# Kernel tuning notes

Hardware: AMD Instinct MI355X
Metric: run time of the kernel (lower is better)

The kernel has to match this reference:

```python
import jax, jax.numpy as jnp
import numpy as np
import math

NUM_HEADS = 16


def setup_inputs() -> dict:
    key = jax.random.key(0)
    ks = jax.random.split(key, 5)
    B, C, H = 2, 2048, 1024
    return {
        "x": jax.random.normal(ks[0], (B, C, H), dtype=jnp.float32),
        "Wqkv_w": jax.random.normal(ks[1], (3 * H, H), dtype=jnp.float32) * (1.0 / math.sqrt(H)),
        "Wqkv_b": jax.random.normal(ks[2], (3 * H,), dtype=jnp.float32) * 0.02,
        "Wo_w": jax.random.normal(ks[3], (H, H), dtype=jnp.float32) * (1.0 / math.sqrt(H)),
        "Wo_b": jax.random.normal(ks[4], (H,), dtype=jnp.float32) * 0.02,
    }


def reference(x, Wqkv_w, Wqkv_b, Wo_w, Wo_b):
    B, C, H = x.shape
    nh = NUM_HEADS
    hd = H // nh
    # QKV projection (torch Linear: x @ W.T + b)
    qkv = x @ Wqkv_w.T + Wqkv_b                      # [B, C, 3H]
    qkv = qkv.reshape(B, C, 3, nh, hd)
    qkv = jnp.transpose(qkv, (2, 0, 3, 1, 4))        # [3, B, nh, C, hd]
    q, k, v = qkv[0], qkv[1], qkv[2]
    scale = 1.0 / math.sqrt(hd)
    att = jnp.einsum('bhqd,bhkd->bhqk', q, k) * scale  # [B, nh, C, C]
    causal = jnp.triu(jnp.ones((C, C), dtype=bool), k=1)  # True above diagonal
    att = jnp.where(causal[None, None], jnp.float32(-jnp.inf), att)
    att = jax.nn.softmax(att, axis=-1)
    # dropout p set to 0 (eval-mode math)
    out = jnp.einsum('bhqk,bhkd->bhqd', att, v)       # [B, nh, C, hd]
    out = jnp.transpose(out, (0, 2, 1, 3)).reshape(B, C, H)
    return out @ Wo_w.T + Wo_b
```

## Files before the change

### kernel.cpp

```cpp
#include <hip/hip_runtime.h>
#include <hip/hip_bf16.h>
#include <math.h>

typedef unsigned short u16;
typedef __attribute__((ext_vector_type(8))) __bf16 bf16x8;
typedef __attribute__((ext_vector_type(4))) float f32x4;
typedef __attribute__((ext_vector_type(8))) unsigned short u16x8;
typedef __attribute__((ext_vector_type(4))) unsigned int u32x4;

__device__ __forceinline__ u16 f2bf(float f) {
  union { float f; unsigned u; } x; x.f = f;
  unsigned r = x.u + 0x7fffu + ((x.u >> 16) & 1u);
  return (u16)(r >> 16);
}

__device__ __forceinline__ void gload16(const u16* g, u16* l) {
  __builtin_amdgcn_global_load_lds(
      (const __attribute__((address_space(1))) void*)g,
      (__attribute__((address_space(3))) void*)l, 16, 0, 0);
}

#define MFMA16(a, b, c) __builtin_amdgcn_mfma_f32_16x16x32_bf16((a), (b), (c), 0, 0, 0)

#define QSCALE 0.18033688011112043f

__global__ __launch_bounds__(256) void cast_all_kernel(
    const float* __restrict__ x, const float* __restrict__ wqkv,
    const float* __restrict__ wo, u16* __restrict__ xb,
    u16* __restrict__ wqb, u16* __restrict__ wob) {
  int i = blockIdx.x * 256 + threadIdx.x;
  const float* src; u16* dst;
  if (i < 1048576)      { src = x;    dst = xb;  }
  else if (i < 1835008) { src = wqkv; dst = wqb; i -= 1048576; }
  else                  { src = wo;   dst = wob; i -= 1835008; }
  f32x4 v = *(const f32x4*)(src + (size_t)i * 4);
  u16 o0 = f2bf(v[0]), o1 = f2bf(v[1]), o2 = f2bf(v[2]), o3 = f2bf(v[3]);
  unsigned lo = (unsigned)o0 | ((unsigned)o1 << 16);
  unsigned hi = (unsigned)o2 | ((unsigned)o3 << 16);
  ((unsigned*)dst)[(size_t)i * 2] = lo;
  ((unsigned*)dst)[(size_t)i * 2 + 1] = hi;
}

__global__ __launch_bounds__(512, 2) void gemm_qkv_kernel(
    const u16* __restrict__ X, const u16* __restrict__ W, const float* __restrict__ bias,
    u16* __restrict__ Qb, u16* __restrict__ Kb, u16* __restrict__ Vb) {
  __shared__ __align__(16) u16 As[2][2][128 * 64];
  __shared__ __align__(16) u16 Bs[2][2][128 * 64];
  const int tid = threadIdx.x;
  const int lane = tid & 63;
  const int wid = tid >> 6;
  const int wm = wid >> 2, wn = wid & 3;
  const int g = lane >> 4, q15 = lane & 15;
  const int m0b = blockIdx.y * 256;
  const int n0b = blockIdx.x * 256;
  const int sA = 2 * ((q15 >> 2) & 1);

  auto stageA = [&](int kt, int h) {
    #pragma unroll
    for (int it = 0; it < 2; ++it) {
      int c = it * 512 + tid;
      int row = c >> 3, kg = c & 7;
      int kgs = kg ^ (2 * ((row >> 2) & 1));
      gload16(X + (size_t)(m0b + h * 128 + row) * 1024 + kt * 64 + kgs * 8,
              &As[kt & 1][h][c * 8]);
    }
  };
  auto stageB = [&](int kt, int h) {
    #pragma unroll
    for (int it = 0; it < 2; ++it) {
      int c = it * 512 + tid;
      int row = c >> 3, kg = c & 7;
      int kgs = kg ^ (2 * ((row >> 2) & 1));
      gload16(W + (size_t)(n0b + h * 128 + row) * 1024 + kt * 64 + kgs * 8,
              &Bs[kt & 1][h][c * 8]);
    }
  };

  f32x4 acc[8][4] = {};

  stageA(0, 0); stageA(0, 1);
  stageB(0, 0); stageB(0, 1);
  stageB(1, 0); stageB(1, 1);
  asm volatile("s_waitcnt vmcnt(4)" ::: "memory");
  __builtin_amdgcn_s_barrier();

  for (int kt = 0; kt < 16; ++kt) {
    const int d = kt & 1;
    const u16* Ah = As[d][wm];
    const u16* Bh = Bs[d][wn >> 1];
    const int rB0 = (wn & 1) * 64;
    bf16x8 bfr[4][2];
    #pragma unroll
    for (int q = 0; q < 4; ++q) {
      bf16x8 afr[2][2];
      if (q == 0) {
        #pragma unroll
        for (int n = 0; n < 4; ++n)
          #pragma unroll
          for (int kk = 0; kk < 2; ++kk) {
            int row = rB0 + n * 16 + q15;
            int kg = (kk * 4 + g) ^ sA;
            bfr[n][kk] = *(const bf16x8*)(Bh + row * 64 + kg * 8);
          }
      }
      #pragma unroll
      for (int p = 0; p < 2; ++p)
        #pragma unroll
        for (int kk = 0; kk < 2; ++kk) {
          int row = (2 * q + p) * 16 + q15;
          int kg = (kk * 4 + g) ^ sA;
          afr[p][kk] = *(const bf16x8*)(Ah + row * 64 + kg * 8);
        }
      if (q == 0)      { if (kt + 1 < 16) stageA(kt + 1, 0); }
      else if (q == 1) { if (kt + 1 < 16) stageA(kt + 1, 1); }
      else if (q == 2) { if (kt + 2 < 16) stageB(kt + 2, 0); }
      else             { if (kt + 2 < 16) stageB(kt + 2, 1); }
      __builtin_amdgcn_s_barrier();
      asm volatile("s_waitcnt lgkmcnt(0)" ::: "memory");
      __builtin_amdgcn_sched_barrier(0);
      __builtin_amdgcn_s_setprio(1);
      #pragma unroll
      for (int kk = 0; kk < 2; ++kk)
        #pragma unroll
        for (int p = 0; p < 2; ++p)
          #pragma unroll
          for (int n = 0; n < 4; ++n)
            acc[2 * q + p][n] = MFMA16(afr[p][kk], bfr[n][kk], acc[2 * q + p][n]);
      __builtin_amdgcn_s_setprio(0);
      if (q == 3) {
        if (kt < 14)       asm volatile("s_waitcnt vmcnt(4)" ::: "memory");
        else if (kt == 14) asm volatile("s_waitcnt vmcnt(0)" ::: "memory");
      }
      __builtin_amdgcn_s_barrier();
    }
  }

  const int which = n0b >> 10;
  const float qs = (which == 0) ? QSCALE : 1.0f;
  u16* __restrict__ dst = (which == 0) ? Qb : (which == 1 ? Kb : Vb);
  #pragma unroll
  for (int n = 0; n < 4; ++n) {
    int gcol = n0b + wn * 64 + n * 16 + q15;
    float bz = bias[gcol];
    int h = (gcol >> 6) & 15, d0 = gcol & 63;
    #pragma unroll
    for (int m = 0; m < 8; ++m)
      #pragma unroll
      for (int j = 0; j < 4; ++j) {
        int grow = m0b + wm * 128 + m * 16 + g * 4 + j;
        int bb = grow >> 11, qq = grow & 2047;
        dst[((size_t)((bb * 16 + h) * 2048 + qq)) * 64 + d0] =
            f2bf((acc[m][n][j] + bz) * qs);
      }
  }
}

__global__ __launch_bounds__(256) void gemm_out_kernel(
    const u16* __restrict__ Ain, const u16* __restrict__ W, const float* __restrict__ bias,
    float* __restrict__ out) {
  __shared__ __align__(16) u16 As[64 * 64];
  __shared__ __align__(16) u16 Bs[128 * 64];
  const int tid = threadIdx.x;
  const int lane = tid & 63;
  const int wc = tid >> 6;
  const int m0 = blockIdx.y * 64;
  const int n0 = blockIdx.x * 128;
  f32x4 acc[4][2] = {};
  for (int k0 = 0; k0 < 1024; k0 += 64) {
    #pragma unroll
    for (int it = 0; it < 2; ++it) {
      int c = it * 256 + tid;
      gload16(Ain + (size_t)(m0 + (c >> 3)) * 1024 + k0 + ((c & 7) << 3), As + c * 8);
    }
    #pragma unroll
    for (int it = 0; it < 4; ++it) {
      int c = it * 256 + tid;
      gload16(W + (size_t)(n0 + (c >> 3)) * 1024 + k0 + ((c & 7) << 3), Bs + c * 8);
    }
    __syncthreads();
    #pragma unroll
    for (int kk = 0; kk < 2; ++kk) {
      bf16x8 a[4], b[2];
      #pragma unroll
      for (int m = 0; m < 4; ++m)
        a[m] = *(const bf16x8*)(As + ((m * 16 + (lane & 15)) * 64 +
                                      kk * 32 + ((lane >> 4) << 3)));
      #pragma unroll
      for (int n = 0; n < 2; ++n)
        b[n] = *(const bf16x8*)(Bs + ((wc * 32 + n * 16 + (lane & 15)) * 64 +
                                      kk * 32 + ((lane >> 4) << 3)));
      #pragma unroll
      for (int m = 0; m < 4; ++m)
        #pragma unroll
        for (int n = 0; n < 2; ++n)
          acc[m][n] = MFMA16(a[m], b[n], acc[m][n]);
    }
    __syncthreads();
  }
  #pragma unroll
  for (int m = 0; m < 4; ++m)
    #pragma unroll
    for (int n = 0; n < 2; ++n)
      #pragma unroll
      for (int j = 0; j < 4; ++j) {
        int row = m0 + m * 16 + ((lane >> 4) << 2) + j;
        int col = n0 + wc * 32 + n * 16 + (lane & 15);
        out[(size_t)row * 1024 + col] = acc[m][n][j] + bias[col];
      }
}

__device__ __forceinline__ void attn_one(
    const u16* __restrict__ Qh, const u16* __restrict__ Kh, const u16* __restrict__ Vh,
    u16* __restrict__ Ob, int bb, int h, int qt,
    u16 (*Ks)[64 * 64], u16 (*Vt)[64 * 64]) {
  const int tid = threadIdx.x, lane = tid & 63, w = tid >> 6;
  const int g = lane >> 4, q15 = lane & 15;

  bf16x8 qf[2];
  const int qrow = qt * 64 + w * 16 + q15;
  #pragma unroll
  for (int kk = 0; kk < 2; ++kk)
    qf[kk] = *(const bf16x8*)(Qh + (size_t)qrow * 64 + kk * 32 + g * 8);

  f32x4 acc_o[4];
  #pragma unroll
  for (int n = 0; n < 4; ++n) acc_o[n] = (f32x4){0.f, 0.f, 0.f, 0.f};
  float m_run = -INFINITY, l_run = 0.f;

  const int nt = qt + 1;

  auto stageK = [&](int t, int buf) {
    #pragma unroll
    for (int it = 0; it < 2; ++it) {
      int c = it * 256 + tid;
      int row = c >> 3, b8 = c & 7;
      gload16(Kh + (size_t)(t * 64 + row) * 64 + ((b8 ^ (row & 7)) << 3),
              Ks[buf] + c * 8);
    }
  };

  stageK(0, 0);
  #pragma unroll
  for (int it = 0; it < 2; ++it) {
    int kloc = it * 32 + (tid >> 3);
    int d0 = (tid & 7) << 3;
    u16x8 v = *(const u16x8*)(Vh + (size_t)kloc * 64 + d0);
    #pragma unroll
    for (int i = 0; i < 8; ++i) {
      int d = d0 + i;
      int fv = (d + (d >> 3)) & 7;
      Vt[0][d * 64 + (((kloc >> 3) ^ fv) << 3) + (kloc & 7)] = v[i];
    }
  }
  __syncthreads();

  for (int t = 0; t < nt; ++t) {
    const int cur = t & 1;
    const bool pre = (t + 1 < nt);
    u16x8 vreg[2];
    if (pre) {
      stageK(t + 1, cur ^ 1);
      #pragma unroll
      for (int it = 0; it < 2; ++it) {
        int kloc = it * 32 + (tid >> 3);
        int d0 = (tid & 7) << 3;
        vreg[it] = *(const u16x8*)(Vh + (size_t)((t + 1) * 64 + kloc) * 64 + d0);
      }
    }

    f32x4 accs[4];
    __builtin_amdgcn_s_setprio(1);
    #pragma unroll
    for (int cb = 0; cb < 4; ++cb) {
      accs[cb] = (f32x4){0.f, 0.f, 0.f, 0.f};
      #pragma unroll
      for (int kk = 0; kk < 2; ++kk) {
        int row = cb * 16 + q15;
        int kblk = kk * 4 + g;
        bf16x8 kf = *(const bf16x8*)(Ks[cur] + row * 64 + ((kblk ^ (row & 7)) << 3));
        accs[cb] = MFMA16(kf, qf[kk], accs[cb]);
      }
    }
    __builtin_amdgcn_s_setprio(0);
    if (t == nt - 1) {
      #pragma unroll
      for (int cb = 0; cb < 4; ++cb)
        #pragma unroll
        for (int j = 0; j < 4; ++j) {
          int kg = t * 64 + cb * 16 + 4 * g + j;
          if (kg > qrow) accs[cb][j] = -INFINITY;
        }
    }

    float mj = accs[0][0];
    #pragma unroll
    for (int cb = 0; cb < 4; ++cb)
      #pragma unroll
      for (int j = 0; j < 4; ++j) mj = fmaxf(mj, accs[cb][j]);
    mj = fmaxf(mj, __shfl_xor(mj, 16));
    mj = fmaxf(mj, __shfl_xor(mj, 32));
    if (!__all(mj - m_run <= 8.0f)) {
      float mn = fmaxf(m_run, mj);
      float sc = exp2f(m_run - mn);
      m_run = mn;
      l_run *= sc;
      float scj[4];
      #pragma unroll
      for (int j = 0; j < 4; ++j) scj[j] = __shfl(sc, 4 * g + j);
      #pragma unroll
      for (int n = 0; n < 4; ++n)
        #pragma unroll
        for (int j = 0; j < 4; ++j) acc_o[n][j] *= scj[j];
    }
    float rs = 0.f;
    #pragma unroll
    for (int cb = 0; cb < 4; ++cb)
      #pragma unroll
      for (int j = 0; j < 4; ++j) {
        float p = exp2f(accs[cb][j] - m_run);
        accs[cb][j] = p;
        rs += p;
      }
    rs += __shfl_xor(rs, 16);
    rs += __shfl_xor(rs, 32);
    l_run += rs;

    unsigned Wp[4][2];
    #pragma unroll
    for (int cb = 0; cb < 4; ++cb)
      #pragma unroll
      for (int hh = 0; hh < 2; ++hh)
        asm("v_cvt_pk_bf16_f32 %0, %1, %2"
            : "=v"(Wp[cb][hh]) : "v"(accs[cb][2 * hh]), "v"(accs[cb][2 * hh + 1]));

    unsigned aw[2][4];
    #pragma unroll
    for (int kk = 0; kk < 2; ++kk)
      #pragma unroll
      for (int iw = 0; iw < 4; ++iw) {
        int srcLane = q15 + ((((g & 1) << 1) + (iw >> 1)) << 4);
        unsigned c0 = __shfl(Wp[2 * kk + 0][iw & 1], srcLane);
        unsigned c1 = __shfl(Wp[2 * kk + 1][iw & 1], srcLane);
        aw[kk][iw] = (g >> 1) ? c1 : c0;
      }
    bf16x8 pa0 = __builtin_bit_cast(bf16x8, (u32x4){aw[0][0], aw[0][1], aw[0][2], aw[0][3]});
    bf16x8 pa1 = __builtin_bit_cast(bf16x8, (u32x4){aw[1][0], aw[1][1], aw[1][2], aw[1][3]});

    __builtin_amdgcn_s_setprio(1);
    #pragma unroll
    for (int n = 0; n < 4; ++n) {
      #pragma unroll
      for (int kk = 0; kk < 2; ++kk) {
        int cblk = kk * 4 + g;
        int d = n * 16 + q15;
        int fv = (d + (d >> 3)) & 7;
        bf16x8 vb = *(const bf16x8*)(Vt[cur] + d * 64 + ((cblk ^ fv) << 3));
        acc_o[n] = MFMA16(kk ? pa1 : pa0, vb, acc_o[n]);
      }
    }
    __builtin_amdgcn_s_setprio(0);

    if (pre) {
      #pragma unroll
      for (int it = 0; it < 2; ++it) {
        int kloc = it * 32 + (tid >> 3);
        int d0 = (tid & 7) << 3;
        #pragma unroll
        for (int i = 0; i < 8; ++i) {
          int d = d0 + i;
          int fv = (d + (d >> 3)) & 7;
          Vt[cur ^ 1][d * 64 + (((kloc >> 3) ^ fv) << 3) + (kloc & 7)] = vreg[it][i];
        }
      }
    }
    __syncthreads();
  }

  float invl = 1.0f / l_run;
  float invj[4];
  #pragma unroll
  for (int j = 0; j < 4; ++j) invj[j] = __shfl(invl, 4 * g + j);
  #pragma unroll
  for (int n = 0; n < 4; ++n)
    #pragma unroll
    for (int j = 0; j < 4; ++j) {
      int qg = qt * 64 + w * 16 + 4 * g + j;
      Ob[((size_t)(bb * 2048 + qg)) * 1024 + h * 64 + n * 16 + q15] =
          f2bf(acc_o[n][j] * invj[j]);
    }
}

__global__ __launch_bounds__(256, 4) void attn_kernel(
    const u16* __restrict__ Qb, const u16* __restrict__ Kb, const u16* __restrict__ Vb,
    u16* __restrict__ Ob) {
  __shared__ __align__(16) u16 Ks[2][64 * 64];
  __shared__ __align__(16) u16 Vt[2][64 * 64];
  const int blk = blockIdx.x;
  const int p = blk & 15;
  const int bh = blk >> 4;
  const size_t base = (size_t)bh * 2048 * 64;
  const int bb = bh >> 4, h = bh & 15;
  attn_one(Qb + base, Kb + base, Vb + base, Ob, bb, h, 31 - p, Ks, Vt);
  attn_one(Qb + base, Kb + base, Vb + base, Ob, bb, h, p, Ks, Vt);
}

extern "C" void kernel_launch(void* const* d_in, const int* in_sizes, int n_in,
                              void* d_out, int out_size, void* d_ws, size_t ws_size,
                              hipStream_t stream) {
  const float* x    = (const float*)d_in[0];
  const float* wqkv = (const float*)d_in[1];
  const float* bqkv = (const float*)d_in[2];
  const float* wo   = (const float*)d_in[3];
  const float* bo   = (const float*)d_in[4];
  float* out = (float*)d_out;

  const size_t MB = 1u << 20;
  char* ws = (char*)d_ws;
  u16* x_bf  = (u16*)(ws);
  u16* wq_bf = (u16*)(ws + 8 * MB);
  u16* wo_bf = (u16*)(ws + 14 * MB);
  u16* q_buf = (u16*)(ws + 16 * MB);
  u16* k_buf = (u16*)(ws + 24 * MB);
  u16* v_buf = (u16*)(ws + 32 * MB);
  u16* a_out = (u16*)(ws + 40 * MB);

  cast_all_kernel<<<8192, 256, 0, stream>>>(x, wqkv, wo, x_bf, wq_bf, wo_bf);

  gemm_qkv_kernel<<<dim3(12, 16), 512, 0, stream>>>(x_bf, wq_bf, bqkv,
                                                    q_buf, k_buf, v_buf);
  attn_kernel<<<512, 256, 0, stream>>>(q_buf, k_buf, v_buf, a_out);
  gemm_out_kernel<<<dim3(8, 64), 256, 0, stream>>>(a_out, wo_bf, bo, out);
}
```

Baseline: 144.7 us.

## Emit V pre-transposed per 64-key tile from QKV GEMM epilogue

The QKV GEMM epilogue for the V columns now stages the output tile through shared memory and writes V in a per-tile transposed layout ([bh][tile][d][key]). The attention kernel can then load V with async global-to-LDS copies just like K, instead of loading into registers and scattering a transpose into LDS every iteration. This removes per-iteration scalar LDS scatter work and register pressure in attention, at the cost of extra syncs and LDS traffic in the GEMM epilogue for a third of its blocks.

```diff
diff --git a/kernel.cpp b/kernel.cpp
--- a/kernel.cpp
+++ b/kernel.cpp
@@ -43,7 +43,7 @@
 
 __global__ __launch_bounds__(512, 2) void gemm_qkv_kernel(
     const u16* __restrict__ X, const u16* __restrict__ W, const float* __restrict__ bias,
-    u16* __restrict__ Qb, u16* __restrict__ Kb, u16* __restrict__ Vb) {
+    u16* __restrict__ Qb, u16* __restrict__ Kb, u16* __restrict__ V2) {
   __shared__ __align__(16) u16 As[2][2][128 * 64];
   __shared__ __align__(16) u16 Bs[2][2][128 * 64];
   const int tid = threadIdx.x;
@@ -136,22 +136,59 @@
   }
 
   const int which = n0b >> 10;
-  const float qs = (which == 0) ? QSCALE : 1.0f;
-  u16* __restrict__ dst = (which == 0) ? Qb : (which == 1 ? Kb : Vb);
-  #pragma unroll
-  for (int n = 0; n < 4; ++n) {
-    int gcol = n0b + wn * 64 + n * 16 + q15;
-    float bz = bias[gcol];
-    int h = (gcol >> 6) & 15, d0 = gcol & 63;
-    #pragma unroll
-    for (int m = 0; m < 8; ++m)
-      #pragma unroll
-      for (int j = 0; j < 4; ++j) {
-        int grow = m0b + wm * 128 + m * 16 + g * 4 + j;
+
+  if (which < 2) {
+    const float qs = (which == 0) ? QSCALE : 1.0f;
+    u16* __restrict__ dst = (which == 0) ? Qb : Kb;
+    #pragma unroll
+    for (int n = 0; n < 4; ++n) {
+      int gcol = n0b + wn * 64 + n * 16 + q15;
+      float bz = bias[gcol];
+      int h = (gcol >> 6) & 15, d0 = gcol & 63;
+      #pragma unroll
+      for (int m = 0; m < 8; ++m)
+        #pragma unroll
+        for (int j = 0; j < 4; ++j) {
+          int grow = m0b + wm * 128 + m * 16 + g * 4 + j;
+          int bb = grow >> 11, qq = grow & 2047;
+          dst[((size_t)((bb * 16 + h) * 2048 + qq)) * 64 + d0] =
+              f2bf((acc[m][n][j] + bz) * qs);
+        }
+    }
+  } else {
+    u16* Ct = &As[0][0][0];
+    #pragma unroll
+    for (int half = 0; half < 2; ++half) {
+      __syncthreads();
+      if ((wn >> 1) == half) {
+        #pragma unroll
+        for (int n = 0; n < 4; ++n) {
+          int c = (wn & 1) * 64 + n * 16 + q15;
+          float bz = bias[n0b + half * 128 + c];
+          #pragma unroll
+          for (int m = 0; m < 8; ++m)
+            #pragma unroll
+            for (int j = 0; j < 4; ++j) {
+              int r = wm * 128 + m * 16 + g * 4 + j;
+              Ct[c * 256 + (r ^ ((c & 15) << 3))] = f2bf(acc[m][n][j] + bz);
+            }
+        }
+      }
+      __syncthreads();
+      #pragma unroll
+      for (int i = 0; i < 8; ++i) {
+        int chunk = i * 512 + tid;
+        int cc = chunk >> 5;
+        int r0 = (chunk & 31) * 8;
+        u16x8 val = *(const u16x8*)(Ct + cc * 256 + (r0 ^ ((cc & 15) << 3)));
+        int gcol = n0b + half * 128 + cc;
+        int h = (gcol >> 6) & 15, d0 = gcol & 63;
+        int grow = m0b + r0;
         int bb = grow >> 11, qq = grow & 2047;
-        dst[((size_t)((bb * 16 + h) * 2048 + qq)) * 64 + d0] =
-            f2bf((acc[m][n][j] + bz) * qs);
-      }
+        int tt = qq >> 6, key = qq & 63;
+        *(u16x8*)(V2 + ((((size_t)(bb * 16 + h) * 32 + tt) * 64 + d0) * 64 + key)) = val;
+      }
+    }
   }
 }
 
@@ -210,9 +247,9 @@
 }
 
 __device__ __forceinline__ void attn_one(
-    const u16* __restrict__ Qh, const u16* __restrict__ Kh, const u16* __restrict__ Vh,
+    const u16* __restrict__ Qh, const u16* __restrict__ Kh, const u16* __restrict__ V2h,
     u16* __restrict__ Ob, int bb, int h, int qt,
-    u16 (*Ks)[64 * 64], u16 (*Vt)[64 * 64]) {
+    u16 (*Ks)[64 * 64], u16 (*Vs)[64 * 64]) {
   const int tid = threadIdx.x, lane = tid & 63, w = tid >> 6;
   const int g = lane >> 4, q15 = lane & 15;
 
@@ -238,35 +275,24 @@
               Ks[buf] + c * 8);
     }
   };
+  auto stageV = [&](int t, int buf) {
+    #pragma unroll
+    for (int it = 0; it < 2; ++it) {
+      int c = it * 256 + tid;
+      int row = c >> 3, b8 = c & 7;
+      gload16(V2h + (size_t)t * 4096 + row * 64 + ((b8 ^ (row & 7)) << 3),
+              Vs[buf] + c * 8);
+    }
+  };
 
   stageK(0, 0);
-  #pragma unroll
-  for (int it = 0; it < 2; ++it) {
-    int kloc = it * 32 + (tid >> 3);
-    int d0 = (tid & 7) << 3;
-    u16x8 v = *(const u16x8*)(Vh + (size_t)kloc * 64 + d0);
-    #pragma unroll
-    for (int i = 0; i < 8; ++i) {
-      int d = d0 + i;
-      int fv = (d + (d >> 3)) & 7;
-      Vt[0][d * 64 + (((kloc >> 3) ^ fv) << 3) + (kloc & 7)] = v[i];
-    }
-  }
+  stageV(0, 0);
   __syncthreads();
 
   for (int t = 0; t < nt; ++t) {
     const int cur = t & 1;
     const bool pre = (t + 1 < nt);
-    u16x8 vreg[2];
-    if (pre) {
-      stageK(t + 1, cur ^ 1);
-      #pragma unroll
-      for (int it = 0; it < 2; ++it) {
-        int kloc = it * 32 + (tid >> 3);
-        int d0 = (tid & 7) << 3;
-        vreg[it] = *(const u16x8*)(Vh + (size_t)((t + 1) * 64 + kloc) * 64 + d0);
-      }
-    }
+    if (pre) { stageK(t + 1, cur ^ 1); stageV(t + 1, cur ^ 1); }
 
     f32x4 accs[4];
     __builtin_amdgcn_s_setprio(1);
@@ -351,28 +377,13 @@
     for (int n = 0; n < 4; ++n) {
       #pragma unroll
       for (int kk = 0; kk < 2; ++kk) {
-        int cblk = kk * 4 + g;
         int d = n * 16 + q15;
-        int fv = (d + (d >> 3)) & 7;
-        bf16x8 vb = *(const bf16x8*)(Vt[cur] + d * 64 + ((cblk ^ fv) << 3));
+        int kblk = kk * 4 + g;
+        bf16x8 vb = *(const bf16x8*)(Vs[cur] + d * 64 + ((kblk ^ (d & 7)) << 3));
         acc_o[n] = MFMA16(kk ? pa1 : pa0, vb, acc_o[n]);
       }
     }
     __builtin_amdgcn_s_setprio(0);
-
-    if (pre) {
-      #pragma unroll
-      for (int it = 0; it < 2; ++it) {
-        int kloc = it * 32 + (tid >> 3);
-        int d0 = (tid & 7) << 3;
-        #pragma unroll
-        for (int i = 0; i < 8; ++i) {
-          int d = d0 + i;
-          int fv = (d + (d >> 3)) & 7;
-          Vt[cur ^ 1][d * 64 + (((kloc >> 3) ^ fv) << 3) + (kloc & 7)] = vreg[it][i];
-        }
-      }
-    }
     __syncthreads();
   }
 
@@ -391,17 +402,17 @@
 }
 
 __global__ __launch_bounds__(256, 4) void attn_kernel(
-    const u16* __restrict__ Qb, const u16* __restrict__ Kb, const u16* __restrict__ Vb,
+    const u16* __restrict__ Qb, const u16* __restrict__ Kb, const u16* __restrict__ V2b,
     u16* __restrict__ Ob) {
   __shared__ __align__(16) u16 Ks[2][64 * 64];
-  __shared__ __align__(16) u16 Vt[2][64 * 64];
+  __shared__ __align__(16) u16 Vs[2][64 * 64];
   const int blk = blockIdx.x;
   const int p = blk & 15;
   const int bh = blk >> 4;
   const size_t base = (size_t)bh * 2048 * 64;
   const int bb = bh >> 4, h = bh & 15;
-  attn_one(Qb + base, Kb + base, Vb + base, Ob, bb, h, 31 - p, Ks, Vt);
-  attn_one(Qb + base, Kb + base, Vb + base, Ob, bb, h, p, Ks, Vt);
+  attn_one(Qb + base, Kb + base, V2b + base, Ob, bb, h, 31 - p, Ks, Vs);
+  attn_one(Qb + base, Kb + base, V2b + base, Ob, bb, h, p, Ks, Vs);
 }
 
 extern "C" void kernel_launch(void* const* d_in, const int* in_sizes, int n_in,
@@ -421,13 +432,13 @@
   u16* wo_bf = (u16*)(ws + 14 * MB);
   u16* q_buf = (u16*)(ws + 16 * MB);
   u16* k_buf = (u16*)(ws + 24 * MB);
-  u16* v_buf = (u16*)(ws + 32 * MB);
+  u16* v2_buf= (u16*)(ws + 32 * MB);
   u16* a_out = (u16*)(ws + 40 * MB);
 
   cast_all_kernel<<<8192, 256, 0, stream>>>(x, wqkv, wo, x_bf, wq_bf, wo_bf);
 
   gemm_qkv_kernel<<<dim3(12, 16), 512, 0, stream>>>(x_bf, wq_bf, bqkv,
-                                                    q_buf, k_buf, v_buf);
-  attn_kernel<<<512, 256, 0, stream>>>(q_buf, k_buf, v_buf, a_out);
+                                                    q_buf, k_buf, v2_buf);
+  attn_kernel<<<512, 256, 0, stream>>>(q_buf, k_buf, v2_buf, a_out);
   gemm_out_kernel<<<dim3(8, 64), 256, 0, stream>>>(a_out, wo_bf, bo, out);
 }
```

Result: faster. 134.7 us (-6.9%).
